# Kernel tuning notes

Measured on AMD Instinct MI355X. Metric: run time of the kernel, lower is better.

Reference implementation:

```python
import jax, jax.numpy as jnp
import numpy as np

WH, WW = 7, 7
N = WH * WW            # 49 tokens per window
DIM = 128
HEADS = 4
HEAD_DIM = DIM // HEADS
SCALE = HEAD_DIM ** -0.5
NW = 1024              # windows per image (224/7)^2
B = 16                 # images
B_ = B * NW


def _relative_position_index():
    ch, cw = np.meshgrid(np.arange(WH), np.arange(WW), indexing='ij')
    coords = np.stack([ch, cw]).reshape(2, -1)          # [2, N]
    rel = coords[:, :, None] - coords[:, None, :]        # [2, N, N]
    rel = rel.transpose(1, 2, 0)
    rel[:, :, 0] += WH - 1
    rel[:, :, 1] += WW - 1
    rel[:, :, 0] *= 2 * WW - 1
    return rel.sum(-1).astype(np.int32)                 # [N, N]


def setup_inputs() -> dict:
    key = jax.random.key(0)
    ks = jax.random.split(key, 5)
    x = jax.random.normal(ks[0], (B_, N, DIM), dtype=jnp.float32)
    mask = jnp.zeros((NW, N, N), dtype=jnp.float32)
    qkv_w = jax.random.normal(ks[1], (3 * DIM, DIM), dtype=jnp.float32) * (DIM ** -0.5)
    qkv_b = jnp.zeros((3 * DIM,), dtype=jnp.float32)
    proj_w = jax.random.normal(ks[2], (DIM, DIM), dtype=jnp.float32) * (DIM ** -0.5)
    proj_b = jnp.zeros((DIM,), dtype=jnp.float32)
    rel_bias_table = jax.random.normal(ks[3], ((2 * WH - 1) * (2 * WW - 1), HEADS), dtype=jnp.float32) * 0.02
    rel_index = jnp.asarray(_relative_position_index())
    return {"x": x, "mask": mask, "qkv_w": qkv_w, "qkv_b": qkv_b,
            "proj_w": proj_w, "proj_b": proj_b,
            "rel_bias_table": rel_bias_table, "rel_index": rel_index}


def reference(x, mask, qkv_w, qkv_b, proj_w, proj_b, rel_bias_table, rel_index):
    Bw, n, c = x.shape
    # fused qkv projection: [B_, N, 3, H, hd]
    qkv = (x @ qkv_w.T + qkv_b).reshape(Bw, n, 3, HEADS, HEAD_DIM)
    qkv = jnp.transpose(qkv, (2, 0, 3, 1, 4))            # [3, B_, H, N, hd]
    q, k, v = qkv[0], qkv[1], qkv[2]
    attn = jnp.einsum('bhnd,bhmd->bhnm', q * SCALE, k)   # [B_, H, N, N]
    # gathered relative position bias: [N, N, H] -> [H, N, N]
    bias = rel_bias_table[rel_index.reshape(-1)].reshape(n, n, HEADS)
    attn = attn + jnp.transpose(bias, (2, 0, 1))[None]
    # additive per-window mask
    nW = mask.shape[0]
    attn = attn.reshape(Bw // nW, nW, HEADS, n, n) + mask[None, :, None]
    attn = jax.nn.softmax(attn.reshape(Bw, HEADS, n, n), axis=-1)
    out = jnp.einsum('bhnm,bhmd->bhnd', attn, v)         # [B_, H, N, hd]
    out = jnp.transpose(out, (0, 2, 1, 3)).reshape(Bw, n, c)
    return out @ proj_w.T + proj_b
```

## Files before the change

### kernel.cpp

```cpp
#include <hip/hip_runtime.h>
#include <hip/hip_bf16.h>


#define NTOK 49
#define DIMC 128
#define HEADS 4
#define NWM  1024
#define SCALE 0.17677669529663687f

typedef __attribute__((ext_vector_type(8))) __bf16 bf16x8;
typedef __attribute__((ext_vector_type(4))) float f32x4;

#define OFF_Q  0
#define OFF_K  12544
#define OFF_P  0
#define OFF_VT 25088
#define OFF_AO 25088
#define SMEM_BYTES 39440

__device__ __forceinline__ unsigned short f2bf(float f) {
  union { float f; unsigned u; } x; x.f = f;
  unsigned r = x.u + 0x7fffu + ((x.u >> 16) & 1u);
  return (unsigned short)(r >> 16);
}

__device__ __forceinline__ unsigned pk2(float a, float b) {
  __hip_bfloat162 t = __float22bfloat162_rn(make_float2(a, b));
  union { __hip_bfloat162 h; unsigned u; } c; c.h = t;
  return c.u;
}

__device__ __forceinline__ f32x4 mfma16(bf16x8 a, bf16x8 b, f32x4 c) {
  return __builtin_amdgcn_mfma_f32_16x16x32_bf16(a, b, c, 0, 0, 0);
}

__device__ __forceinline__ bf16x8 zero8() {
  bf16x8 z;
#pragma unroll
  for (int j = 0; j < 8; ++j) z[j] = (__bf16)0.f;
  return z;
}

__global__ void winattn_prep(const float* __restrict__ qkv_w,
                             const float* __restrict__ proj_w,
                             const float* __restrict__ table,
                             const int* __restrict__ ridx,
                             unsigned short* __restrict__ qkv_wb,
                             unsigned short* __restrict__ proj_wb,
                             float* __restrict__ bias_g) {
  int i = blockIdx.x * 256 + threadIdx.x;
  if (i < 384 * DIMC) qkv_wb[i] = f2bf(qkv_w[i]);
  if (i < DIMC * DIMC) proj_wb[i] = f2bf(proj_w[i]);
  if (i < HEADS * 64 * 64) {
    int h = i >> 12, n = (i >> 6) & 63, m = i & 63;
    float v = -1e30f;
    if (n < NTOK && m < NTOK) v = table[ridx[n * NTOK + m] * HEADS + h];
    bias_g[i] = v;
  }
}

__launch_bounds__(256, 4)
__global__ void winattn_main(const float* __restrict__ x,
                             const float* __restrict__ mask,
                             const unsigned short* __restrict__ qkv_wb,
                             const float* __restrict__ qkv_b,
                             const unsigned short* __restrict__ proj_wb,
                             const float* __restrict__ proj_b,
                             const float* __restrict__ bias_g,
                             float* __restrict__ out) {
  __shared__ char smem[SMEM_BYTES] __attribute__((aligned(128)));
  const int tid  = threadIdx.x;
  const int w    = blockIdx.x;
  const int lane = tid & 63;
  const int wid  = tid >> 6;
  const int lr   = lane & 15;
  const int lg   = lane >> 4;
  const f32x4 fzero = {0.f, 0.f, 0.f, 0.f};

  const float* xw = x + (size_t)w * (NTOK * DIMC);

  if (tid == 0)
    *reinterpret_cast<uint4*>(smem + SMEM_BYTES - 16) = make_uint4(0u, 0u, 0u, 0u);

  bf16x8 af[4][4];
#pragma unroll
  for (int mt = 0; mt < 4; ++mt)
#pragma unroll
    for (int kk = 0; kk < 4; ++kk) {
      int n = mt * 16 + lr;
      bool pad = (n > 48);
      int nc = pad ? 48 : n;
      const float* src = xw + nc * DIMC + kk * 32 + lg * 8;
      float4 v0 = *reinterpret_cast<const float4*>(src);
      float4 v1 = *reinterpret_cast<const float4*>(src + 4);
      uint4 d;
      d.x = pk2(v0.x, v0.y); d.y = pk2(v0.z, v0.w);
      d.z = pk2(v1.x, v1.y); d.w = pk2(v1.z, v1.w);
      union { uint4 u; bf16x8 b; } cvt; cvt.u = d;
      af[mt][kk] = pad ? zero8() : cvt.b;
    }

  {
    const int cb = wid * 96;
#pragma unroll
    for (int nt = 0; nt < 6; ++nt) {
      const int o = cb + nt * 16 + lr;
      const unsigned short* wrow = qkv_wb + o * DIMC;
      bf16x8 bf[4];
#pragma unroll
      for (int kk = 0; kk < 4; ++kk)
        bf[kk] = *reinterpret_cast<const bf16x8*>(wrow + kk * 32 + lg * 8);
      f32x4 acc[4];
#pragma unroll
      for (int mt = 0; mt < 4; ++mt) acc[mt] = fzero;
#pragma unroll
      for (int kk = 0; kk < 4; ++kk)
#pragma unroll
        for (int mt = 0; mt < 4; ++mt)
          acc[mt] = mfma16(af[mt][kk], bf[kk], acc[mt]);
      const float bq = qkv_b[o];
      const int s  = o >> 7;
      const int h2 = (o & 127) >> 5;
      const int d  = o & 31;
#pragma unroll
      for (int mt = 0; mt < 4; ++mt)
#pragma unroll
        for (int r = 0; r < 4; ++r) {
          const int n = mt * 16 + lg * 4 + r;
          const unsigned short bv = f2bf(acc[mt][r] + bq);
          if (s == 2) {
            if (n < 56)
              *reinterpret_cast<unsigned short*>(
                  smem + OFF_VT + (h2 * 32 + d) * 112 + n * 2) = bv;
          } else if (n < NTOK) {
            int base = (s == 0) ? OFF_Q : OFF_K;
            int mb = (d * 2) ^ ((n & 3) << 4);
            *reinterpret_cast<unsigned short*>(
                smem + base + (h2 * NTOK + n) * 64 + mb) = bv;
          }
        }
    }
  }
  __syncthreads();

  const int h = wid;
  {
    bf16x8 qf[4], kf[4];
#pragma unroll
    for (int mt = 0; mt < 4; ++mt) {
      int n = mt * 16 + lr; if (n > 48) n = 48;
      int mb = (lg * 16) ^ ((n & 3) << 4);
      qf[mt] = *reinterpret_cast<const bf16x8*>(smem + OFF_Q + (h * NTOK + n) * 64 + mb);
    }
#pragma unroll
    for (int nt = 0; nt < 4; ++nt) {
      int m = nt * 16 + lr; if (m > 48) m = 48;
      int mb = (lg * 16) ^ ((m & 3) << 4);
      kf[nt] = *reinterpret_cast<const bf16x8*>(smem + OFF_K + (h * NTOK + m) * 64 + mb);
    }
    f32x4 sc[4][4];
#pragma unroll
    for (int mt = 0; mt < 4; ++mt)
#pragma unroll
      for (int nt = 0; nt < 4; ++nt)
        sc[mt][nt] = mfma16(qf[mt], kf[nt], fzero);

    const float* bgh = bias_g + h * 4096;
    const float* mw  = mask + (size_t)(w & (NWM - 1)) * (NTOK * NTOK);
#pragma unroll
    for (int mt = 0; mt < 4; ++mt)
#pragma unroll
      for (int r = 0; r < 4; ++r) {
        const int n  = mt * 16 + lg * 4 + r;
        const int nc = (n > 48) ? 48 : n;
#pragma unroll
        for (int nt = 0; nt < 4; ++nt) {
          const int m  = nt * 16 + lr;
          const int mc = (m > 48) ? 48 : m;
          sc[mt][nt][r] = sc[mt][nt][r] * SCALE + bgh[n * 64 + m] + mw[nc * NTOK + mc];
        }
      }
    __syncthreads();

#pragma unroll
    for (int mt = 0; mt < 4; ++mt)
#pragma unroll
      for (int r = 0; r < 4; ++r) {
        float mx = sc[mt][0][r];
#pragma unroll
        for (int nt = 1; nt < 4; ++nt) mx = fmaxf(mx, sc[mt][nt][r]);
        mx = fmaxf(mx, __shfl_xor(mx, 1, 16));
        mx = fmaxf(mx, __shfl_xor(mx, 2, 16));
        mx = fmaxf(mx, __shfl_xor(mx, 4, 16));
        mx = fmaxf(mx, __shfl_xor(mx, 8, 16));
        float e[4]; float sum = 0.f;
#pragma unroll
        for (int nt = 0; nt < 4; ++nt) { e[nt] = __expf(sc[mt][nt][r] - mx); sum += e[nt]; }
        sum += __shfl_xor(sum, 1, 16);
        sum += __shfl_xor(sum, 2, 16);
        sum += __shfl_xor(sum, 4, 16);
        sum += __shfl_xor(sum, 8, 16);
        const float inv = __builtin_amdgcn_rcpf(sum);
        const int n = mt * 16 + lg * 4 + r;
        if (n < NTOK) {
#pragma unroll
          for (int nt = 0; nt < 4; ++nt) {
            const int m = nt * 16 + lr;
            int mb = (m * 2) ^ ((n & 7) << 4);
            *reinterpret_cast<unsigned short*>(smem + OFF_P + (h * NTOK + n) * 128 + mb) =
                f2bf(e[nt] * inv);
          }
        }
      }
  }

  {
    bf16x8 pa[4][2], vb[2][2];
#pragma unroll
    for (int mt = 0; mt < 4; ++mt)
#pragma unroll
      for (int kk = 0; kk < 2; ++kk) {
        int n = mt * 16 + lr; if (n > 48) n = 48;
        int mb = (kk * 64 + lg * 16) ^ ((n & 7) << 4);
        pa[mt][kk] = *reinterpret_cast<const bf16x8*>(smem + OFF_P + (h * NTOK + n) * 128 + mb);
      }
#pragma unroll
    for (int dt = 0; dt < 2; ++dt)
#pragma unroll
      for (int kk = 0; kk < 2; ++kk) {
        const int d = dt * 16 + lr;
        vb[dt][kk] = *reinterpret_cast<const bf16x8*>(
            smem + OFF_VT + (h * 32 + d) * 112 + kk * 64 + 16 * lg);
      }
    f32x4 oc[4][2];
#pragma unroll
    for (int mt = 0; mt < 4; ++mt)
#pragma unroll
      for (int dt = 0; dt < 2; ++dt) oc[mt][dt] = fzero;
#pragma unroll
    for (int kk = 0; kk < 2; ++kk)
#pragma unroll
      for (int mt = 0; mt < 4; ++mt)
#pragma unroll
        for (int dt = 0; dt < 2; ++dt)
          oc[mt][dt] = mfma16(pa[mt][kk], vb[dt][kk], oc[mt][dt]);
    __syncthreads();
#pragma unroll
    for (int mt = 0; mt < 4; ++mt)
#pragma unroll
      for (int dt = 0; dt < 2; ++dt)
#pragma unroll
        for (int r = 0; r < 4; ++r) {
          const int n = mt * 16 + lg * 4 + r;
          if (n < NTOK) {
            const int c = h * 32 + dt * 16 + lr;
            int mb = (c * 2) ^ ((n & 7) << 4);
            *reinterpret_cast<unsigned short*>(smem + OFF_AO + n * 256 + mb) =
                f2bf(oc[mt][dt][r]);
          }
        }
  }
  __syncthreads();

  {
    bf16x8 aof[4][4];
#pragma unroll
    for (int mt = 0; mt < 4; ++mt)
#pragma unroll
      for (int kk = 0; kk < 4; ++kk) {
        int n = mt * 16 + lr; if (n > 48) n = 48;
        int s16 = 4 * kk + lg;
        aof[mt][kk] = *reinterpret_cast<const bf16x8*>(
            smem + OFF_AO + n * 256 + (((s16 & 8) | ((s16 ^ (n & 7)) & 7)) << 4));
      }
    float* ow = out + (size_t)w * (NTOK * DIMC);
#pragma unroll
    for (int ct = 0; ct < 2; ++ct) {
      const int c = (wid * 2 + ct) * 16 + lr;
      const unsigned short* wrow = proj_wb + c * DIMC;
      bf16x8 wb[4];
#pragma unroll
      for (int kk = 0; kk < 4; ++kk)
        wb[kk] = *reinterpret_cast<const bf16x8*>(wrow + kk * 32 + lg * 8);
      f32x4 acc[4];
#pragma unroll
      for (int mt = 0; mt < 4; ++mt) acc[mt] = fzero;
#pragma unroll
      for (int kk = 0; kk < 4; ++kk)
#pragma unroll
        for (int mt = 0; mt < 4; ++mt)
          acc[mt] = mfma16(aof[mt][kk], wb[kk], acc[mt]);
      const float bp = proj_b[c];
#pragma unroll
      for (int mt = 0; mt < 4; ++mt)
#pragma unroll
        for (int r = 0; r < 4; ++r) {
          const int n = mt * 16 + lg * 4 + r;
          if (n < NTOK) ow[n * DIMC + c] = acc[mt][r] + bp;
        }
    }
  }
}

extern "C" void kernel_launch(void* const* d_in, const int* in_sizes, int n_in,
                              void* d_out, int out_size, void* d_ws, size_t ws_size,
                              hipStream_t stream) {
  const float* x      = (const float*)d_in[0];
  const float* mask   = (const float*)d_in[1];
  const float* qkv_w  = (const float*)d_in[2];
  const float* qkv_b  = (const float*)d_in[3];
  const float* proj_w = (const float*)d_in[4];
  const float* proj_b = (const float*)d_in[5];
  const float* table  = (const float*)d_in[6];
  const int*   ridx   = (const int*)d_in[7];

  unsigned short* qkv_wb  = (unsigned short*)d_ws;
  unsigned short* proj_wb = qkv_wb + 384 * DIMC;
  float*          bias_g  = (float*)(proj_wb + DIMC * DIMC);

  winattn_prep<<<192, 256, 0, stream>>>(qkv_w, proj_w, table, ridx,
                                        qkv_wb, proj_wb, bias_g);

  const int nwin = in_sizes[0] / (NTOK * DIMC);
  winattn_main<<<nwin, 256, 0, stream>>>(x, mask, qkv_wb, qkv_b, proj_wb,
                                         proj_b, bias_g, (float*)d_out);
}
```

Before: 571.0 us.

## Make each wave compute its own head's QKV, keep V in registers, shrink LDS

Each wave now computes the Q, K and V columns for its own head instead of an arbitrary 96-column slice. Q and K go into a per-head private LDS region, and V is rearranged into MFMA B-operand fragments held in registers via cross-lane shuffles. This removes the block-wide barriers between the QKV projection and attention, removes the V-transpose round trip through LDS, and reduces LDS from about 39KB to 25KB so the launch bound can request 5 blocks per CU. The tradeoff is more register pressure from the held V fragments plus extra shuffle instructions, and the per-head LDS regions now overlap where Q/K/P are reused.

```diff
diff --git a/kernel.cpp b/kernel.cpp
--- a/kernel.cpp
+++ b/kernel.cpp
@@ -11,12 +11,7 @@
 typedef __attribute__((ext_vector_type(8))) __bf16 bf16x8;
 typedef __attribute__((ext_vector_type(4))) float f32x4;
 
-#define OFF_Q  0
-#define OFF_K  12544
-#define OFF_P  0
-#define OFF_VT 25088
-#define OFF_AO 25088
-#define SMEM_BYTES 39440
+#define SMEM_BYTES 25088
 
 __device__ __forceinline__ unsigned short f2bf(float f) {
   union { float f; unsigned u; } x; x.f = f;
@@ -59,7 +54,7 @@
   }
 }
 
-__launch_bounds__(256, 4)
+__launch_bounds__(256, 5)
 __global__ void winattn_main(const float* __restrict__ x,
                              const float* __restrict__ mask,
                              const unsigned short* __restrict__ qkv_wb,
@@ -75,12 +70,11 @@
   const int wid  = tid >> 6;
   const int lr   = lane & 15;
   const int lg   = lane >> 4;
+  const int h    = wid;
+  const int hb   = h * 6272;
   const f32x4 fzero = {0.f, 0.f, 0.f, 0.f};
 
   const float* xw = x + (size_t)w * (NTOK * DIMC);
-
-  if (tid == 0)
-    *reinterpret_cast<uint4*>(smem + SMEM_BYTES - 16) = make_uint4(0u, 0u, 0u, 0u);
 
   bf16x8 af[4][4];
 #pragma unroll
@@ -100,63 +94,83 @@
       af[mt][kk] = pad ? zero8() : cvt.b;
     }
 
-  {
-    const int cb = wid * 96;
-#pragma unroll
-    for (int nt = 0; nt < 6; ++nt) {
-      const int o = cb + nt * 16 + lr;
-      const unsigned short* wrow = qkv_wb + o * DIMC;
-      bf16x8 bf[4];
-#pragma unroll
-      for (int kk = 0; kk < 4; ++kk)
-        bf[kk] = *reinterpret_cast<const bf16x8*>(wrow + kk * 32 + lg * 8);
-      f32x4 acc[4];
-#pragma unroll
-      for (int mt = 0; mt < 4; ++mt) acc[mt] = fzero;
-#pragma unroll
-      for (int kk = 0; kk < 4; ++kk)
-#pragma unroll
-        for (int mt = 0; mt < 4; ++mt)
-          acc[mt] = mfma16(af[mt][kk], bf[kk], acc[mt]);
-      const float bq = qkv_b[o];
-      const int s  = o >> 7;
-      const int h2 = (o & 127) >> 5;
-      const int d  = o & 31;
+  bf16x8 vb[2][2];
+#pragma unroll
+  for (int t = 0; t < 6; ++t) {
+    const int sec  = t >> 1;
+    const int half = t & 1;
+    const int o0   = sec * 128 + 32 * h + 16 * half;
+    const unsigned short* wrow = qkv_wb + (o0 + lr) * DIMC;
+    bf16x8 wf[4];
+#pragma unroll
+    for (int kk = 0; kk < 4; ++kk)
+      wf[kk] = *reinterpret_cast<const bf16x8*>(wrow + kk * 32 + 8 * lg);
+    f32x4 acc[4];
+#pragma unroll
+    for (int mt = 0; mt < 4; ++mt) acc[mt] = fzero;
+#pragma unroll
+    for (int kk = 0; kk < 4; ++kk)
+#pragma unroll
+      for (int mt = 0; mt < 4; ++mt)
+        acc[mt] = mfma16(af[mt][kk], wf[kk], acc[mt]);
+    const float bq = qkv_b[o0 + lr];
+    const int d = 16 * half + lr;
+    if (sec < 2) {
+      const int base = hb + ((sec == 1) ? 3136 : 0);
 #pragma unroll
       for (int mt = 0; mt < 4; ++mt)
 #pragma unroll
         for (int r = 0; r < 4; ++r) {
           const int n = mt * 16 + lg * 4 + r;
-          const unsigned short bv = f2bf(acc[mt][r] + bq);
-          if (s == 2) {
-            if (n < 56)
-              *reinterpret_cast<unsigned short*>(
-                  smem + OFF_VT + (h2 * 32 + d) * 112 + n * 2) = bv;
-          } else if (n < NTOK) {
-            int base = (s == 0) ? OFF_Q : OFF_K;
+          if (n < NTOK) {
             int mb = (d * 2) ^ ((n & 3) << 4);
-            *reinterpret_cast<unsigned short*>(
-                smem + base + (h2 * NTOK + n) * 64 + mb) = bv;
+            *reinterpret_cast<unsigned short*>(smem + base + n * 64 + mb) =
+                f2bf(acc[mt][r] + bq);
           }
         }
-    }
-  }
-  __syncthreads();
-
-  const int h = wid;
+    } else {
+      uint2 pk[4];
+#pragma unroll
+      for (int mt = 0; mt < 4; ++mt) {
+        pk[mt].x = pk2(acc[mt][0] + bq, acc[mt][1] + bq);
+        pk[mt].y = pk2(acc[mt][2] + bq, acc[mt][3] + bq);
+      }
+      const int srcLow  = lr + ((lg & 1) ? 32 : 0);
+      const int srcHigh = srcLow + 16;
+      const bool hiSel  = (lg >> 1) != 0;
+#pragma unroll
+      for (int kk = 0; kk < 2; ++kk) {
+        unsigned a0x = __shfl(pk[kk * 2].x, srcLow);
+        unsigned a0y = __shfl(pk[kk * 2].y, srcLow);
+        unsigned a1x = __shfl(pk[kk * 2 + 1].x, srcLow);
+        unsigned a1y = __shfl(pk[kk * 2 + 1].y, srcLow);
+        unsigned b0x = __shfl(pk[kk * 2].x, srcHigh);
+        unsigned b0y = __shfl(pk[kk * 2].y, srcHigh);
+        unsigned b1x = __shfl(pk[kk * 2 + 1].x, srcHigh);
+        unsigned b1y = __shfl(pk[kk * 2 + 1].y, srcHigh);
+        union { uint4 u; bf16x8 b; } cvt;
+        cvt.u.x = hiSel ? a1x : a0x;
+        cvt.u.y = hiSel ? a1y : a0y;
+        cvt.u.z = hiSel ? b1x : b0x;
+        cvt.u.w = hiSel ? b1y : b0y;
+        vb[half][kk] = cvt.b;
+      }
+    }
+  }
+
   {
     bf16x8 qf[4], kf[4];
 #pragma unroll
     for (int mt = 0; mt < 4; ++mt) {
       int n = mt * 16 + lr; if (n > 48) n = 48;
       int mb = (lg * 16) ^ ((n & 3) << 4);
-      qf[mt] = *reinterpret_cast<const bf16x8*>(smem + OFF_Q + (h * NTOK + n) * 64 + mb);
+      qf[mt] = *reinterpret_cast<const bf16x8*>(smem + hb + n * 64 + mb);
     }
 #pragma unroll
     for (int nt = 0; nt < 4; ++nt) {
       int m = nt * 16 + lr; if (m > 48) m = 48;
       int mb = (lg * 16) ^ ((m & 3) << 4);
-      kf[nt] = *reinterpret_cast<const bf16x8*>(smem + OFF_K + (h * NTOK + m) * 64 + mb);
+      kf[nt] = *reinterpret_cast<const bf16x8*>(smem + hb + 3136 + m * 64 + mb);
     }
     f32x4 sc[4][4];
 #pragma unroll
@@ -180,7 +194,6 @@
           sc[mt][nt][r] = sc[mt][nt][r] * SCALE + bgh[n * 64 + m] + mw[nc * NTOK + mc];
         }
       }
-    __syncthreads();
 
 #pragma unroll
     for (int mt = 0; mt < 4; ++mt)
@@ -207,7 +220,7 @@
           for (int nt = 0; nt < 4; ++nt) {
             const int m = nt * 16 + lr;
             int mb = (m * 2) ^ ((n & 7) << 4);
-            *reinterpret_cast<unsigned short*>(smem + OFF_P + (h * NTOK + n) * 128 + mb) =
+            *reinterpret_cast<unsigned short*>(smem + hb + n * 128 + mb) =
                 f2bf(e[nt] * inv);
           }
         }
@@ -215,22 +228,14 @@
   }
 
   {
-    bf16x8 pa[4][2], vb[2][2];
+    bf16x8 pa[4][2];
 #pragma unroll
     for (int mt = 0; mt < 4; ++mt)
 #pragma unroll
       for (int kk = 0; kk < 2; ++kk) {
         int n = mt * 16 + lr; if (n > 48) n = 48;
         int mb = (kk * 64 + lg * 16) ^ ((n & 7) << 4);
-        pa[mt][kk] = *reinterpret_cast<const bf16x8*>(smem + OFF_P + (h * NTOK + n) * 128 + mb);
-      }
-#pragma unroll
-    for (int dt = 0; dt < 2; ++dt)
-#pragma unroll
-      for (int kk = 0; kk < 2; ++kk) {
-        const int d = dt * 16 + lr;
-        vb[dt][kk] = *reinterpret_cast<const bf16x8*>(
-            smem + OFF_VT + (h * 32 + d) * 112 + kk * 64 + 16 * lg);
+        pa[mt][kk] = *reinterpret_cast<const bf16x8*>(smem + hb + n * 128 + mb);
       }
     f32x4 oc[4][2];
 #pragma unroll
@@ -255,7 +260,7 @@
           if (n < NTOK) {
             const int c = h * 32 + dt * 16 + lr;
             int mb = (c * 2) ^ ((n & 7) << 4);
-            *reinterpret_cast<unsigned short*>(smem + OFF_AO + n * 256 + mb) =
+            *reinterpret_cast<unsigned short*>(smem + n * 256 + mb) =
                 f2bf(oc[mt][dt][r]);
           }
         }
@@ -271,7 +276,7 @@
         int n = mt * 16 + lr; if (n > 48) n = 48;
         int s16 = 4 * kk + lg;
         aof[mt][kk] = *reinterpret_cast<const bf16x8*>(
-            smem + OFF_AO + n * 256 + (((s16 & 8) | ((s16 ^ (n & 7)) & 7)) << 4));
+            smem + n * 256 + (((s16 & 8) | ((s16 ^ (n & 7)) & 7)) << 4));
       }
     float* ow = out + (size_t)w * (NTOK * DIMC);
 #pragma unroll
```

After: 1.035 ms. 1.81x slower.
